# Kernel tuning notes

Hardware: AMD Instinct MI355X
Metric: run time of the kernel (lower is better)

The kernel has to match this reference:

```python
import jax, jax.numpy as jnp
import numpy as np

B, S, T, D, H, DF, E = 16, 1024, 512, 512, 8, 2048, 4
DH = D // H
EPS = 1e-5


def setup_inputs() -> dict:
    key = jax.random.key(0)
    ks = iter(jax.random.split(key, 64))

    def nrm(shape, scale=0.02):
        return jax.random.normal(next(ks), shape, dtype=jnp.float32) * scale

    inp = {
        "x": jax.random.normal(next(ks), (B, S, D), dtype=jnp.float32),
        "cross": jax.random.normal(next(ks), (B, T, D), dtype=jnp.float32),
    }
    for p in ("sa", "ca"):
        for w in ("wq", "wk", "wv", "wo"):
            inp[f"{p}_{w}"] = nrm((D, D))
            inp[f"{p}_b{w[1]}"] = jnp.zeros((D,), jnp.float32)
    inp["gate_w"] = nrm((D, E))
    inp["gate_b"] = jnp.zeros((E,), jnp.float32)
    inp["exp_w1"] = nrm((E, D, DF))
    inp["exp_b1"] = jnp.zeros((E, DF), jnp.float32)
    inp["exp_w2"] = nrm((E, DF, D))
    inp["exp_b2"] = jnp.zeros((E, D), jnp.float32)
    for i in (1, 2, 3):
        inp[f"n{i}_g"] = jnp.ones((D,), jnp.float32)
        inp[f"n{i}_b"] = jnp.zeros((D,), jnp.float32)
    return inp


def layer_norm(x, g, b):
    m = x.mean(-1, keepdims=True)
    v = x.var(-1, keepdims=True)
    return (x - m) * jax.lax.rsqrt(v + EPS) * g + b


def mha(q_in, kv_in, wq, bq, wk, bk, wv, bv, wo, bo, causal):
    Bq, Sq, _ = q_in.shape
    Sk = kv_in.shape[1]
    q = (q_in @ wq + bq).reshape(Bq, Sq, H, DH)
    k = (kv_in @ wk + bk).reshape(Bq, Sk, H, DH)
    v = (kv_in @ wv + bv).reshape(Bq, Sk, H, DH)
    scores = jnp.einsum('bshd,bthd->bhst', q, k) / jnp.sqrt(jnp.float32(DH))
    if causal:
        mask = jnp.tril(jnp.ones((Sq, Sk), dtype=bool))
        scores = jnp.where(mask, scores, jnp.float32(-1e9))
    attn = jax.nn.softmax(scores, axis=-1)
    out = jnp.einsum('bhst,bthd->bshd', attn, v).reshape(Bq, Sq, D)
    return out @ wo + bo


def moe_ffn(x, gw, gb, w1, b1, w2, b2):
    gates = jax.nn.softmax(x @ gw + gb, axis=-1)            # [B,S,E]
    h = jax.nn.relu(jnp.einsum('bsd,edf->bsef', x, w1) + b1)  # [B,S,E,DF]
    yo = jnp.einsum('bsef,efd->bsed', h, w2) + b2            # [B,S,E,D]
    y = jnp.einsum('bse,bsed->bsd', gates, yo)
    imp = gates.mean((0, 1))                                 # importance per expert
    aux = jnp.float32(E) * jnp.sum(imp * imp)                # load-balance penalty
    return y, aux


def reference(x, cross,
              sa_wq, sa_bq, sa_wk, sa_bk, sa_wv, sa_bv, sa_wo, sa_bo,
              ca_wq, ca_bq, ca_wk, ca_bk, ca_wv, ca_bv, ca_wo, ca_bo,
              gate_w, gate_b, exp_w1, exp_b1, exp_w2, exp_b2,
              n1_g, n1_b, n2_g, n2_b, n3_g, n3_b):
    # dropout is identity in eval mode
    x = x + mha(x, x, sa_wq, sa_bq, sa_wk, sa_bk, sa_wv, sa_bv, sa_wo, sa_bo, causal=True)
    x = layer_norm(x, n1_g, n1_b)
    x = x + mha(x, cross, ca_wq, ca_bq, ca_wk, ca_bk, ca_wv, ca_bv, ca_wo, ca_bo, causal=False)
    x = layer_norm(x, n2_g, n2_b)
    y, aux_loss = moe_ffn(x, gate_w, gate_b, exp_w1, exp_b1, exp_w2, exp_b2)
    out = layer_norm(x + y, n3_g, n3_b)
    return out, aux_loss
```

## Files before the change

### kernel.cpp

```cpp
#include <hip/hip_runtime.h>
#include <stdint.h>
#include <stddef.h>

typedef unsigned short bf16u;
typedef __attribute__((ext_vector_type(8))) short short8;
typedef __attribute__((ext_vector_type(4))) float f32x4;

__device__ __forceinline__ bf16u f2bf(float f) {
  union { float f; unsigned u; } v; v.f = f;
  unsigned r = v.u + 0x7FFFu + ((v.u >> 16) & 1u);
  return (bf16u)(r >> 16);
}

#define GL16(g, l) __builtin_amdgcn_global_load_lds( \
    (const __attribute__((address_space(1))) unsigned int*)(g), \
    (__attribute__((address_space(3))) unsigned int*)(l), 16, 0, 0)

enum { EPI_BF16 = 0, EPI_RELU_GATE = 1, EPI_QKV = 2, EPI_RES = 3, EPI_F32ACC = 4, EPI_KV = 5 };

template<int EPI>
__global__ __launch_bounds__(256, 3) void gemm_k(
    const bf16u* __restrict__ A, int LDA,
    const bf16u* __restrict__ BT, int LDB,
    const float* __restrict__ bias, const float* __restrict__ res,
    const float* __restrict__ gates,
    bf16u* __restrict__ o1, bf16u* __restrict__ o2, bf16u* __restrict__ o3,
    float* __restrict__ of,
    int N, int K, int slog, int egate0, int firste)
{
  __shared__ bf16u Ab[2][128 * 32];
  __shared__ bf16u Bb[2][128 * 32];
  const int tid = threadIdx.x, lane = tid & 63, w = tid >> 6;
  const int wm = w >> 1, wn = w & 1;
  const int cpx = gridDim.x >> 3;
  const int bid = (blockIdx.x & 7) * cpx + (blockIdx.x >> 3);
  const int nbt = N >> 7;
  const int mt = bid / nbt, nt = bid - mt * nbt;
  const int bm = mt << 7, bn = nt << 7;

  const int srow = lane >> 2;
  const int scol = (lane & 3) << 3;
  const bf16u* ap0 = A + (size_t)(bm + w * 16 + srow) * LDA + scol;
  const bf16u* ap1 = ap0 + (size_t)64 * LDA;
  const bf16u* bp0 = BT + (size_t)(bn + w * 16 + srow) * LDB + scol;
  const bf16u* bp1 = bp0 + (size_t)64 * LDB;

  f32x4 acc[4][4] = {};
  const int NT = K >> 5;

  GL16(ap0, &Ab[0][w * 512]);
  GL16(ap1, &Ab[0][(4 + w) * 512]);
  GL16(bp0, &Bb[0][w * 512]);
  GL16(bp1, &Bb[0][(4 + w) * 512]);
  __syncthreads();

  const int rl = lane & 15, kg = (lane >> 4) << 3;
  int cur = 0;
  for (int kt = 0; kt < NT; ++kt) {
    if (kt + 1 < NT) {
      const int ko = (kt + 1) << 5;
      const int nb = cur ^ 1;
      GL16(ap0 + ko, &Ab[nb][w * 512]);
      GL16(ap1 + ko, &Ab[nb][(4 + w) * 512]);
      GL16(bp0 + ko, &Bb[nb][w * 512]);
      GL16(bp1 + ko, &Bb[nb][(4 + w) * 512]);
    }
    short8 af[4], bfv[4];
    #pragma unroll
    for (int i = 0; i < 4; ++i)
      af[i] = *(const short8*)&Ab[cur][(wm * 64 + i * 16 + rl) * 32 + kg];
    #pragma unroll
    for (int j = 0; j < 4; ++j)
      bfv[j] = *(const short8*)&Bb[cur][(wn * 64 + j * 16 + rl) * 32 + kg];
    #pragma unroll
    for (int i = 0; i < 4; ++i)
      #pragma unroll
      for (int j = 0; j < 4; ++j)
        acc[i][j] = __builtin_amdgcn_mfma_f32_16x16x32_bf16(af[i], bfv[j], acc[i][j], 0, 0, 0);
    __syncthreads();
    cur ^= 1;
  }

  const int r0 = bm + wm * 64, c0 = bn + wn * 64;
  const int rsub = (lane >> 4) << 2;
  #pragma unroll
  for (int j = 0; j < 4; ++j) {
    const int col = c0 + j * 16 + rl;
    const float bs = bias ? bias[col] : 0.f;
    #pragma unroll
    for (int i = 0; i < 4; ++i) {
      const f32x4 v = acc[i][j];
      #pragma unroll
      for (int jj = 0; jj < 4; ++jj) {
        const int row = r0 + i * 16 + rsub + jj;
        const float val = v[jj] + bs;
        if (EPI == EPI_BF16) {
          o1[(size_t)row * N + col] = f2bf(val);
        } else if (EPI == EPI_RELU_GATE) {
          const float g = gates[(size_t)row * 4 + egate0 + (col >> 11)];
          o1[(size_t)row * N + col] = f2bf(g * (val > 0.f ? val : 0.f));
        } else if (EPI == EPI_QKV) {
          if (col < 512) o1[(size_t)row * 512 + col] = f2bf(val);
          else if (col < 1024) o2[(size_t)row * 512 + col - 512] = f2bf(val);
          else {
            const int c = col - 1024;
            const int b_ = row >> slog, t_ = row & ((1 << slog) - 1);
            o3[(((size_t)(b_ * 8 + (c >> 6)) << 6) + (size_t)(c & 63)) * ((size_t)1 << slog) + t_] = f2bf(val);
          }
        } else if (EPI == EPI_KV) {
          if (col < 512) o2[(size_t)row * 512 + col] = f2bf(val);
          else {
            const int c = col - 512;
            const int b_ = row >> slog, t_ = row & ((1 << slog) - 1);
            o3[(((size_t)(b_ * 8 + (c >> 6)) << 6) + (size_t)(c & 63)) * ((size_t)1 << slog) + t_] = f2bf(val);
          }
        } else if (EPI == EPI_RES) {
          of[(size_t)row * N + col] = res[(size_t)row * N + col] + val;
        } else {
          const size_t oi = (size_t)row * N + col;
          of[oi] = firste ? val : (of[oi] + val);
        }
      }
    }
  }
}

template<bool CAUSAL>
__global__ __launch_bounds__(256, 4) void attn_k(
    const bf16u* __restrict__ Q, const bf16u* __restrict__ Kg,
    const bf16u* __restrict__ VT, bf16u* __restrict__ O,
    int Sq, int Sk)
{
  __shared__ bf16u Kl[2][64 * 64];
  __shared__ bf16u Vl[2][64 * 64];
  __shared__ bf16u Pl[64 * 64];
  const int nqt = Sq >> 6;
  const int cpx = gridDim.x >> 3;
  const int bid = (blockIdx.x & 7) * cpx + (blockIdx.x >> 3);
  const int bh = bid / nqt;
  int qt = bid - bh * nqt;
  if (CAUSAL) qt = nqt - 1 - qt;
  const int b = bh >> 3, h = bh & 7;
  const int tid = threadIdx.x, lane = tid & 63, w = tid >> 6;
  const int rl = lane & 15, g4 = lane >> 4;

  const int qrow = qt * 64 + w * 16 + rl;
  const bf16u* qp = Q + (size_t)(b * Sq + qrow) * 512 + h * 64 + g4 * 8;
  const short8 qf0 = *(const short8*)qp;
  const short8 qf1 = *(const short8*)(qp + 32);

  f32x4 oacc[4] = {};
  float ml = -1e30f, ll = 0.f;
  const int KT = CAUSAL ? (qt + 1) : (Sk >> 6);

  const int str = tid >> 2, stc = tid & 3;
  const int sw_st = (str & 7) << 4;
  const bf16u* kq = Kg + (size_t)(b * Sk + str) * 512 + h * 64 + stc * 8;
  const bf16u* vq = VT + (size_t)(bh * 64 + str) * Sk + stc * 8;
  const int lo0 = str * 128 + ((stc * 16) ^ sw_st);
  const int lo1 = str * 128 + ((stc * 16 + 64) ^ sw_st);

  const int qr = w * 16 + rl;
  char* const pbase = (char*)Pl + qr * 128;
  const int swq = (qr & 7) << 4;

  {
    const short8 k0 = *(const short8*)kq;
    const short8 k1 = *(const short8*)(kq + 32);
    const short8 v0 = *(const short8*)vq;
    const short8 v1 = *(const short8*)(vq + 32);
    *(short8*)((char*)Kl[0] + lo0) = k0;
    *(short8*)((char*)Kl[0] + lo1) = k1;
    *(short8*)((char*)Vl[0] + lo0) = v0;
    *(short8*)((char*)Vl[0] + lo1) = v1;
  }
  __syncthreads();

  int cur = 0;
  for (int kt = 0; kt < KT; ++kt) {
    short8 nk0, nk1, nv0, nv1;
    const bool pre = (kt + 1 < KT);
    if (pre) {
      const bf16u* ks = kq + (size_t)(kt + 1) * 64 * 512;
      const bf16u* vs = vq + (kt + 1) * 64;
      nk0 = *(const short8*)ks;
      nk1 = *(const short8*)(ks + 32);
      nv0 = *(const short8*)vs;
      nv1 = *(const short8*)(vs + 32);
    }

    const bf16u* Kc = Kl[cur];
    const bf16u* Vc = Vl[cur];
    f32x4 st[4] = {};
    #pragma unroll
    for (int mi = 0; mi < 4; ++mi) {
      const int kr = mi * 16 + rl;
      const char* kb_ = (const char*)Kc + kr * 128;
      const int sw = (kr & 7) << 4;
      const short8 kf0 = *(const short8*)(kb_ + ((g4 * 16) ^ sw));
      const short8 kf1 = *(const short8*)(kb_ + ((g4 * 16 + 64) ^ sw));
      st[mi] = __builtin_amdgcn_mfma_f32_16x16x32_bf16(kf0, qf0, st[mi], 0, 0, 0);
      st[mi] = __builtin_amdgcn_mfma_f32_16x16x32_bf16(kf1, qf1, st[mi], 0, 0, 0);
    }

    const float SC = 0.125f * 1.44269504f;
    float sv[16];
    float pm = -1e30f;
    if (CAUSAL && kt == qt) {
      const int qg = qt * 64 + qr;
      #pragma unroll
      for (int mi = 0; mi < 4; ++mi)
        #pragma unroll
        for (int jj = 0; jj < 4; ++jj) {
          float s = st[mi][jj] * SC;
          const int kgi = kt * 64 + mi * 16 + g4 * 4 + jj;
          if (kgi > qg) s = -1e30f;
          sv[mi * 4 + jj] = s;
          pm = fmaxf(pm, s);
        }
    } else {
      #pragma unroll
      for (int mi = 0; mi < 4; ++mi)
        #pragma unroll
        for (int jj = 0; jj < 4; ++jj) {
          const float s = st[mi][jj] * SC;
          sv[mi * 4 + jj] = s;
          pm = fmaxf(pm, s);
        }
    }
    pm = fmaxf(pm, __shfl_xor(pm, 16));
    pm = fmaxf(pm, __shfl_xor(pm, 32));
    const float mnew = fmaxf(ml, pm);
    const float alpha = exp2f(ml - mnew);
    float ps = 0.f;
    bf16u pb[16];
    #pragma unroll
    for (int ii = 0; ii < 16; ++ii) {
      const float p = exp2f(sv[ii] - mnew);
      ps += p;
      pb[ii] = f2bf(p);
    }
    ps += __shfl_xor(ps, 16);
    ps += __shfl_xor(ps, 32);
    ll = ll * alpha + ps;
    ml = mnew;

    #pragma unroll
    for (int jj = 0; jj < 4; ++jj) {
      const float aj = __shfl(alpha, g4 * 4 + jj);
      #pragma unroll
      for (int ni = 0; ni < 4; ++ni) oacc[ni][jj] *= aj;
    }

    #pragma unroll
    for (int mi = 0; mi < 4; ++mi) {
      #pragma unroll
      for (int jp = 0; jp < 2; ++jp) {
        const unsigned pk = (unsigned)pb[mi * 4 + jp * 2] | ((unsigned)pb[mi * 4 + jp * 2 + 1] << 16);
        const int kx2 = mi * 32 + g4 * 8 + jp * 4;
        *(unsigned*)(pbase + (kx2 ^ swq)) = pk;
      }
    }
    asm volatile("s_waitcnt lgkmcnt(0)" ::: "memory");
    #pragma unroll
    for (int ks = 0; ks < 2; ++ks) {
      const short8 pf = *(const short8*)(pbase + ((g4 * 16 + ks * 64) ^ swq));
      #pragma unroll
      for (int ni = 0; ni < 4; ++ni) {
        const int vr = ni * 16 + rl;
        const short8 vf = *(const short8*)((const char*)Vc + vr * 128 + ((g4 * 16 + ks * 64) ^ ((vr & 7) << 4)));
        oacc[ni] = __builtin_amdgcn_mfma_f32_16x16x32_bf16(pf, vf, oacc[ni], 0, 0, 0);
      }
    }

    if (pre) {
      const int nb = cur ^ 1;
      *(short8*)((char*)Kl[nb] + lo0) = nk0;
      *(short8*)((char*)Kl[nb] + lo1) = nk1;
      *(short8*)((char*)Vl[nb] + lo0) = nv0;
      *(short8*)((char*)Vl[nb] + lo1) = nv1;
    }
    __syncthreads();
    cur ^= 1;
  }

  #pragma unroll
  for (int jj = 0; jj < 4; ++jj) {
    const float lj = __shfl(ll, g4 * 4 + jj);
    const float inv = 1.f / lj;
    const int row = qt * 64 + w * 16 + g4 * 4 + jj;
    #pragma unroll
    for (int ni = 0; ni < 4; ++ni)
      O[(size_t)(b * Sq + row) * 512 + h * 64 + ni * 16 + rl] = f2bf(oacc[ni][jj] * inv);
  }
}

template<bool ADD, bool BOUT, bool GATE>
__global__ __launch_bounds__(256, 4) void ln_k(
    const float* __restrict__ X, const float* __restrict__ Y,
    const float* __restrict__ gam, const float* __restrict__ bet,
    float* __restrict__ outf, bf16u* __restrict__ outb,
    const float* __restrict__ gw, const float* __restrict__ gb,
    float* __restrict__ gates, float* __restrict__ imp)
{
  __shared__ float sh[4];
  const int tid = threadIdx.x;
  if (GATE) {
    if (tid < 4) sh[tid] = 0.f;
    __syncthreads();
  }
  const int row = blockIdx.x * 4 + (tid >> 6);
  const int lane = tid & 63;
  const float* xp = X + (size_t)row * 512 + lane * 8;
  float v[8];
  {
    const float4 t0 = *(const float4*)xp;
    const float4 t1 = *(const float4*)(xp + 4);
    v[0] = t0.x; v[1] = t0.y; v[2] = t0.z; v[3] = t0.w;
    v[4] = t1.x; v[5] = t1.y; v[6] = t1.z; v[7] = t1.w;
  }
  if (ADD) {
    const float* yp = Y + (size_t)row * 512 + lane * 8;
    const float4 t0 = *(const float4*)yp;
    const float4 t1 = *(const float4*)(yp + 4);
    v[0] += t0.x; v[1] += t0.y; v[2] += t0.z; v[3] += t0.w;
    v[4] += t1.x; v[5] += t1.y; v[6] += t1.z; v[7] += t1.w;
  }
  float s = 0.f, q = 0.f;
  #pragma unroll
  for (int i = 0; i < 8; ++i) { s += v[i]; q += v[i] * v[i]; }
  #pragma unroll
  for (int off = 1; off < 64; off <<= 1) {
    s += __shfl_xor(s, off);
    q += __shfl_xor(q, off);
  }
  const float mean = s * (1.f / 512.f);
  const float var = q * (1.f / 512.f) - mean * mean;
  const float rs = rsqrtf(var + 1e-5f);
  float o[8];
  #pragma unroll
  for (int i = 0; i < 8; ++i)
    o[i] = (v[i] - mean) * rs * gam[lane * 8 + i] + bet[lane * 8 + i];
  float* op = outf + (size_t)row * 512 + lane * 8;
  *(float4*)op = make_float4(o[0], o[1], o[2], o[3]);
  *(float4*)(op + 4) = make_float4(o[4], o[5], o[6], o[7]);
  if (BOUT) {
    union { bf16u u[8]; short8 v8; } pk;
    #pragma unroll
    for (int i = 0; i < 8; ++i) pk.u[i] = f2bf(o[i]);
    *(short8*)(outb + (size_t)row * 512 + lane * 8) = pk.v8;
  }
  if (GATE) {
    float a0 = 0.f, a1 = 0.f, a2 = 0.f, a3 = 0.f;
    #pragma unroll
    for (int i = 0; i < 8; ++i) {
      const float4 wv = *(const float4*)(gw + (lane * 8 + i) * 4);
      a0 += o[i] * wv.x; a1 += o[i] * wv.y; a2 += o[i] * wv.z; a3 += o[i] * wv.w;
    }
    #pragma unroll
    for (int off = 1; off < 64; off <<= 1) {
      a0 += __shfl_xor(a0, off); a1 += __shfl_xor(a1, off);
      a2 += __shfl_xor(a2, off); a3 += __shfl_xor(a3, off);
    }
    if (lane == 0) {
      a0 += gb[0]; a1 += gb[1]; a2 += gb[2]; a3 += gb[3];
      const float m = fmaxf(fmaxf(a0, a1), fmaxf(a2, a3));
      const float e0 = exp2f((a0 - m) * 1.44269504f);
      const float e1 = exp2f((a1 - m) * 1.44269504f);
      const float e2 = exp2f((a2 - m) * 1.44269504f);
      const float e3 = exp2f((a3 - m) * 1.44269504f);
      const float inv = 1.f / (e0 + e1 + e2 + e3);
      float* gr = gates + (size_t)row * 4;
      const float g0 = e0 * inv, g1 = e1 * inv, g2 = e2 * inv, g3 = e3 * inv;
      gr[0] = g0; gr[1] = g1; gr[2] = g2; gr[3] = g3;
      atomicAdd(&sh[0], g0); atomicAdd(&sh[1], g1);
      atomicAdd(&sh[2], g2); atomicAdd(&sh[3], g3);
    }
    __syncthreads();
    if (tid < 4) atomicAdd(&imp[tid], sh[tid]);
  }
}

__global__ __launch_bounds__(256, 4) void ln_final_k(
    const float* __restrict__ X, const float* __restrict__ Y,
    const float* __restrict__ gates, const float* __restrict__ b2,
    const float* __restrict__ gam, const float* __restrict__ bet,
    float* __restrict__ outf, const float* __restrict__ imp,
    float* __restrict__ auxout)
{
  if (blockIdx.x == 0 && threadIdx.x == 0) {
    float s = 0.f;
    #pragma unroll
    for (int e = 0; e < 4; ++e) { const float v = imp[e] * (1.f / 16384.f); s += v * v; }
    auxout[0] = 4.f * s;
  }
  const int row = blockIdx.x * 4 + (threadIdx.x >> 6);
  const int lane = threadIdx.x & 63;
  const float4 gv4 = *(const float4*)(gates + (size_t)row * 4);
  float v[8];
  {
    const float* xp = X + (size_t)row * 512 + lane * 8;
    const float* yp = Y + (size_t)row * 512 + lane * 8;
    const float4 t0 = *(const float4*)xp;
    const float4 t1 = *(const float4*)(xp + 4);
    const float4 u0 = *(const float4*)yp;
    const float4 u1 = *(const float4*)(yp + 4);
    v[0] = t0.x + u0.x; v[1] = t0.y + u0.y; v[2] = t0.z + u0.z; v[3] = t0.w + u0.w;
    v[4] = t1.x + u1.x; v[5] = t1.y + u1.y; v[6] = t1.z + u1.z; v[7] = t1.w + u1.w;
  }
  #pragma unroll
  for (int e = 0; e < 4; ++e) {
    const float ge = e == 0 ? gv4.x : e == 1 ? gv4.y : e == 2 ? gv4.z : gv4.w;
    const float4 b0 = *(const float4*)(b2 + e * 512 + lane * 8);
    const float4 b1 = *(const float4*)(b2 + e * 512 + lane * 8 + 4);
    v[0] += ge * b0.x; v[1] += ge * b0.y; v[2] += ge * b0.z; v[3] += ge * b0.w;
    v[4] += ge * b1.x; v[5] += ge * b1.y; v[6] += ge * b1.z; v[7] += ge * b1.w;
  }
  float s = 0.f, q = 0.f;
  #pragma unroll
  for (int i = 0; i < 8; ++i) { s += v[i]; q += v[i] * v[i]; }
  #pragma unroll
  for (int off = 1; off < 64; off <<= 1) {
    s += __shfl_xor(s, off);
    q += __shfl_xor(q, off);
  }
  const float mean = s * (1.f / 512.f);
  const float var = q * (1.f / 512.f) - mean * mean;
  const float rs = rsqrtf(var + 1e-5f);
  float* op = outf + (size_t)row * 512 + lane * 8;
  float o[8];
  #pragma unroll
  for (int i = 0; i < 8; ++i)
    o[i] = (v[i] - mean) * rs * gam[lane * 8 + i] + bet[lane * 8 + i];
  *(float4*)op = make_float4(o[0], o[1], o[2], o[3]);
  *(float4*)(op + 4) = make_float4(o[4], o[5], o[6], o[7]);
}

__global__ __launch_bounds__(256, 4) void conv_k(const float* __restrict__ in, bf16u* __restrict__ out) {
  const size_t i = ((size_t)blockIdx.x * 256 + threadIdx.x) * 8;
  const float4 a = *(const float4*)(in + i);
  const float4 b = *(const float4*)(in + i + 4);
  union { bf16u u[8]; short8 v; } pk;
  pk.u[0] = f2bf(a.x); pk.u[1] = f2bf(a.y); pk.u[2] = f2bf(a.z); pk.u[3] = f2bf(a.w);
  pk.u[4] = f2bf(b.x); pk.u[5] = f2bf(b.y); pk.u[6] = f2bf(b.z); pk.u[7] = f2bf(b.w);
  *(short8*)(out + i) = pk.v;
}

struct P8 { const float* w[8]; };

__global__ __launch_bounds__(256, 4) void trans8_k(
    P8 ps, bf16u* __restrict__ WT0, int K, int N)
{
  const float* W = ps.w[blockIdx.z];
  bf16u* WT = WT0 + (size_t)blockIdx.z * K * N;
  __shared__ float t[32][33];
  const int tx = threadIdx.x & 31, ty = threadIdx.x >> 5;
  const int n0 = blockIdx.x * 32, k0 = blockIdx.y * 32;
  #pragma unroll
  for (int i = 0; i < 4; ++i)
    t[ty + i * 8][tx] = W[(size_t)(k0 + ty + i * 8) * N + n0 + tx];
  __syncthreads();
  #pragma unroll
  for (int i = 0; i < 4; ++i)
    WT[(size_t)(n0 + ty + i * 8) * K + k0 + tx] = f2bf(t[tx][ty + i * 8]);
}

__global__ __launch_bounds__(256, 4) void trans_s_k(
    const float* __restrict__ W0, size_t wstride,
    bf16u* __restrict__ WT0, size_t tstride, int K, int N)
{
  const float* W = W0 + (size_t)blockIdx.z * wstride;
  bf16u* WT = WT0 + (size_t)blockIdx.z * tstride;
  __shared__ float t[32][33];
  const int tx = threadIdx.x & 31, ty = threadIdx.x >> 5;
  const int n0 = blockIdx.x * 32, k0 = blockIdx.y * 32;
  #pragma unroll
  for (int i = 0; i < 4; ++i)
    t[ty + i * 8][tx] = W[(size_t)(k0 + ty + i * 8) * N + n0 + tx];
  __syncthreads();
  #pragma unroll
  for (int i = 0; i < 4; ++i)
    WT[(size_t)(n0 + ty + i * 8) * K + k0 + tx] = f2bf(t[tx][ty + i * 8]);
}

extern "C" void kernel_launch(void* const* d_in, const int* in_sizes, int n_in,
                              void* d_out, int out_size, void* d_ws, size_t ws_size,
                              hipStream_t stream)
{
  const int B = 16, S = 1024, T = 512, D = 512, DF = 2048, E = 4;
  const int M = B * S;
  const int Mc = B * T;
  (void)in_sizes; (void)n_in; (void)out_size;

  const float* x      = (const float*)d_in[0];
  const float* cross  = (const float*)d_in[1];
  const float* gate_w = (const float*)d_in[18];
  const float* gate_b = (const float*)d_in[19];
  const float* exp_w1 = (const float*)d_in[20];
  const float* exp_b1 = (const float*)d_in[21];
  const float* exp_w2 = (const float*)d_in[22];
  const float* exp_b2 = (const float*)d_in[23];

  char* p = (char*)d_ws;
  auto alloc = [&](size_t bytes) -> char* {
    char* r = p;
    p += (bytes + 255) & ~(size_t)255;
    return r;
  };
  bf16u* w1T   = (bf16u*)alloc((size_t)E * DF * D * 2);
  bf16u* w2T   = (bf16u*)alloc((size_t)D * E * DF * 2);
  float* xf    = (float*)alloc((size_t)M * D * 4);
  bf16u* x2b   = (bf16u*)alloc((size_t)M * D * 2);
  float* gates = (float*)alloc((size_t)M * 4 * 4);
  float* imp   = (float*)alloc(256);
  float* y     = (float*)alloc((size_t)M * D * 4);
  float* qkvb  = (float*)alloc(1536 * 4);
  float* kvb   = (float*)alloc(1024 * 4);

  char* upool = p;
  bf16u* xb  = (bf16u*)upool;
  bf16u* crb = xb  + (size_t)M * D;
  bf16u* wT  = crb + (size_t)Mc * D;
  bf16u* qb  = wT  + (size_t)8 * D * D;
  bf16u* kb  = qb  + (size_t)M * D;
  bf16u* vTb = kb  + (size_t)M * D;
  bf16u* ao  = vTb + (size_t)M * D;
  const size_t attnPool = ((size_t)M * D * 5 + (size_t)Mc * D + (size_t)8 * D * D) * 2;
  bf16u* hbuf = (bf16u*)upool;
  const size_t persistent = (size_t)(upool - (char*)d_ws);
  const size_t perE = (size_t)M * DF * 2;
  const size_t rem = ws_size > persistent ? ws_size - persistent : 0;
  const int EC = (rem >= 4 * perE && rem >= attnPool) ? 4
               : (rem >= 2 * perE && rem >= attnPool) ? 2 : 1;

  hipMemsetAsync(imp, 0, 32, stream);
  hipMemcpyAsync(qkvb,        d_in[3], 512 * 4, hipMemcpyDeviceToDevice, stream);
  hipMemcpyAsync(qkvb + 512,  d_in[5], 512 * 4, hipMemcpyDeviceToDevice, stream);
  hipMemcpyAsync(qkvb + 1024, d_in[7], 512 * 4, hipMemcpyDeviceToDevice, stream);
  hipMemcpyAsync(kvb,         d_in[13], 512 * 4, hipMemcpyDeviceToDevice, stream);
  hipMemcpyAsync(kvb + 512,   d_in[15], 512 * 4, hipMemcpyDeviceToDevice, stream);

  conv_k<<<(M * D) / 2048, 256, 0, stream>>>(x, xb);
  conv_k<<<(Mc * D) / 2048, 256, 0, stream>>>(cross, crb);
  {
    P8 ps;
    for (int i = 0; i < 8; ++i) ps.w[i] = (const float*)d_in[2 + 2 * i];
    trans8_k<<<dim3(D / 32, D / 32, 8), 256, 0, stream>>>(ps, wT, D, D);
  }
  trans_s_k<<<dim3(DF / 32, D / 32, 4), 256, 0, stream>>>(
      exp_w1, (size_t)D * DF, w1T, (size_t)DF * D, D, DF);
  trans_s_k<<<dim3(D / 32, (E * DF) / 32, 1), 256, 0, stream>>>(
      exp_w2, 0, w2T, 0, E * DF, D);

  const int gATT = B * 8 * (S / 64);

  gemm_k<EPI_QKV><<<(M / 128) * 12, 256, 0, stream>>>(
      xb, 512, wT, 512, qkvb, nullptr, nullptr, qb, kb, vTb, nullptr, 1536, 512, 10, 0, 0);
  attn_k<true><<<gATT, 256, 0, stream>>>(qb, kb, vTb, ao, S, S);
  gemm_k<EPI_RES><<<(M / 128) * 4, 256, 0, stream>>>(
      ao, 512, wT + 3 * (size_t)D * D, 512, (const float*)d_in[9], x, nullptr,
      nullptr, nullptr, nullptr, xf, 512, 512, 0, 0, 0);
  ln_k<false, true, false><<<M / 4, 256, 0, stream>>>(
      xf, nullptr, (const float*)d_in[24], (const float*)d_in[25], xf, x2b,
      nullptr, nullptr, nullptr, nullptr);

  gemm_k<EPI_BF16><<<(M / 128) * 4, 256, 0, stream>>>(
      x2b, 512, wT + 4 * (size_t)D * D, 512, (const float*)d_in[11], nullptr, nullptr,
      qb, nullptr, nullptr, nullptr, 512, 512, 0, 0, 0);
  gemm_k<EPI_KV><<<(Mc / 128) * 8, 256, 0, stream>>>(
      crb, 512, wT + 5 * (size_t)D * D, 512, kvb, nullptr, nullptr,
      nullptr, kb, vTb, nullptr, 1024, 512, 9, 0, 0);
  attn_k<false><<<gATT, 256, 0, stream>>>(qb, kb, vTb, ao, S, T);
  gemm_k<EPI_RES><<<(M / 128) * 4, 256, 0, stream>>>(
      ao, 512, wT + 7 * (size_t)D * D, 512, (const float*)d_in[17], xf, nullptr,
      nullptr, nullptr, nullptr, xf, 512, 512, 0, 0, 0);
  ln_k<false, true, true><<<M / 4, 256, 0, stream>>>(
      xf, nullptr, (const float*)d_in[26], (const float*)d_in[27], xf, x2b,
      gate_w, gate_b, gates, imp);

  const int NC = E / EC;
  const int Nh = EC * DF;
  for (int c = 0; c < NC; ++c) {
    gemm_k<EPI_RELU_GATE><<<(M / 128) * (Nh / 128), 256, 0, stream>>>(
        x2b, 512, w1T + (size_t)c * Nh * D, 512, exp_b1 + (size_t)c * Nh, nullptr, gates,
        hbuf, nullptr, nullptr, nullptr, Nh, 512, 0, c * EC, 0);
    gemm_k<EPI_F32ACC><<<(M / 128) * 4, 256, 0, stream>>>(
        hbuf, Nh, w2T + (size_t)c * Nh, E * DF, nullptr, nullptr, nullptr,
        nullptr, nullptr, nullptr, y, 512, Nh, 0, 0, c == 0 ? 1 : 0);
  }
  ln_final_k<<<M / 4, 256, 0, stream>>>(
      xf, y, gates, exp_b2, (const float*)d_in[28], (const float*)d_in[29],
      (float*)d_out, imp, (float*)d_out + (size_t)M * D);
}
```

Before: 869.4 us.

## Keep residual stream in bf16 and raise MFMA wave priority in attention

Stores the residual activations between layers as bf16 instead of fp32. The residual GEMM epilogues now emit bf16, the LayerNorm kernels read bf16 and write only a bf16 output, and a new EPI_RESB epilogue adds a bf16 residual. This removes the fp32 residual writes and reads and the dual-format LN outputs, cutting memory traffic between kernels. It also wraps the attention MFMA blocks in s_setprio so the matrix-multiply sections get scheduling priority. The risk is lower accuracy in the residual path, with bf16 rounding applied before each LayerNorm and the final output.

Measured after the change: 888.8 us. +2.2%, slower.

```diff
diff --git a/kernel.cpp b/kernel.cpp
--- a/kernel.cpp
+++ b/kernel.cpp
@@ -11,19 +11,23 @@
   unsigned r = v.u + 0x7FFFu + ((v.u >> 16) & 1u);
   return (bf16u)(r >> 16);
 }
+__device__ __forceinline__ float bf2f(bf16u u) {
+  union { unsigned u; float f; } v; v.u = (unsigned)u << 16; return v.f;
+}
 
 #define GL16(g, l) __builtin_amdgcn_global_load_lds( \
     (const __attribute__((address_space(1))) unsigned int*)(g), \
     (__attribute__((address_space(3))) unsigned int*)(l), 16, 0, 0)
 
-enum { EPI_BF16 = 0, EPI_RELU_GATE = 1, EPI_QKV = 2, EPI_RES = 3, EPI_F32ACC = 4, EPI_KV = 5 };
+enum { EPI_BF16 = 0, EPI_RELU_GATE = 1, EPI_QKV = 2, EPI_RES = 3, EPI_RESB = 4,
+       EPI_F32ACC = 5, EPI_KV = 6 };
 
 template<int EPI>
 __global__ __launch_bounds__(256, 3) void gemm_k(
     const bf16u* __restrict__ A, int LDA,
     const bf16u* __restrict__ BT, int LDB,
     const float* __restrict__ bias, const float* __restrict__ res,
-    const float* __restrict__ gates,
+    const bf16u* __restrict__ resb, const float* __restrict__ gates,
     bf16u* __restrict__ o1, bf16u* __restrict__ o2, bf16u* __restrict__ o3,
     float* __restrict__ of,
     int N, int K, int slog, int egate0, int firste)
@@ -115,7 +119,9 @@
             o3[(((size_t)(b_ * 8 + (c >> 6)) << 6) + (size_t)(c & 63)) * ((size_t)1 << slog) + t_] = f2bf(val);
           }
         } else if (EPI == EPI_RES) {
-          of[(size_t)row * N + col] = res[(size_t)row * N + col] + val;
+          o1[(size_t)row * N + col] = f2bf(res[(size_t)row * N + col] + val);
+        } else if (EPI == EPI_RESB) {
+          o1[(size_t)row * N + col] = f2bf(bf2f(resb[(size_t)row * N + col]) + val);
         } else {
           const size_t oi = (size_t)row * N + col;
           of[oi] = firste ? val : (of[oi] + val);
@@ -192,6 +198,7 @@
     const bf16u* Kc = Kl[cur];
     const bf16u* Vc = Vl[cur];
     f32x4 st[4] = {};
+    __builtin_amdgcn_s_setprio(1);
     #pragma unroll
     for (int mi = 0; mi < 4; ++mi) {
       const int kr = mi * 16 + rl;
@@ -202,6 +209,7 @@
       st[mi] = __builtin_amdgcn_mfma_f32_16x16x32_bf16(kf0, qf0, st[mi], 0, 0, 0);
       st[mi] = __builtin_amdgcn_mfma_f32_16x16x32_bf16(kf1, qf1, st[mi], 0, 0, 0);
     }
+    __builtin_amdgcn_s_setprio(0);
 
     const float SC = 0.125f * 1.44269504f;
     float sv[16];
@@ -262,6 +270,7 @@
       }
     }
     asm volatile("s_waitcnt lgkmcnt(0)" ::: "memory");
+    __builtin_amdgcn_s_setprio(1);
     #pragma unroll
     for (int ks = 0; ks < 2; ++ks) {
       const short8 pf = *(const short8*)(pbase + ((g4 * 16 + ks * 64) ^ swq));
@@ -272,6 +281,7 @@
         oacc[ni] = __builtin_amdgcn_mfma_f32_16x16x32_bf16(pf, vf, oacc[ni], 0, 0, 0);
       }
     }
+    __builtin_amdgcn_s_setprio(0);
 
     if (pre) {
       const int nb = cur ^ 1;
@@ -295,11 +305,11 @@
   }
 }
 
-template<bool ADD, bool BOUT, bool GATE>
+template<bool GATE>
 __global__ __launch_bounds__(256, 4) void ln_k(
-    const float* __restrict__ X, const float* __restrict__ Y,
+    const bf16u* __restrict__ X,
     const float* __restrict__ gam, const float* __restrict__ bet,
-    float* __restrict__ outf, bf16u* __restrict__ outb,
+    bf16u* __restrict__ outb,
     const float* __restrict__ gw, const float* __restrict__ gb,
     float* __restrict__ gates, float* __restrict__ imp)
 {
@@ -311,21 +321,10 @@
   }
   const int row = blockIdx.x * 4 + (tid >> 6);
   const int lane = tid & 63;
-  const float* xp = X + (size_t)row * 512 + lane * 8;
+  const short8 xv = *(const short8*)(X + (size_t)row * 512 + lane * 8);
   float v[8];
-  {
-    const float4 t0 = *(const float4*)xp;
-    const float4 t1 = *(const float4*)(xp + 4);
-    v[0] = t0.x; v[1] = t0.y; v[2] = t0.z; v[3] = t0.w;
-    v[4] = t1.x; v[5] = t1.y; v[6] = t1.z; v[7] = t1.w;
-  }
-  if (ADD) {
-    const float* yp = Y + (size_t)row * 512 + lane * 8;
-    const float4 t0 = *(const float4*)yp;
-    const float4 t1 = *(const float4*)(yp + 4);
-    v[0] += t0.x; v[1] += t0.y; v[2] += t0.z; v[3] += t0.w;
-    v[4] += t1.x; v[5] += t1.y; v[6] += t1.z; v[7] += t1.w;
-  }
+  #pragma unroll
+  for (int i = 0; i < 8; ++i) v[i] = bf2f((bf16u)xv[i]);
   float s = 0.f, q = 0.f;
   #pragma unroll
   for (int i = 0; i < 8; ++i) { s += v[i]; q += v[i] * v[i]; }
@@ -341,15 +340,10 @@
   #pragma unroll
   for (int i = 0; i < 8; ++i)
     o[i] = (v[i] - mean) * rs * gam[lane * 8 + i] + bet[lane * 8 + i];
-  float* op = outf + (size_t)row * 512 + lane * 8;
-  *(float4*)op = make_float4(o[0], o[1], o[2], o[3]);
-  *(float4*)(op + 4) = make_float4(o[4], o[5], o[6], o[7]);
-  if (BOUT) {
-    union { bf16u u[8]; short8 v8; } pk;
-    #pragma unroll
-    for (int i = 0; i < 8; ++i) pk.u[i] = f2bf(o[i]);
-    *(short8*)(outb + (size_t)row * 512 + lane * 8) = pk.v8;
-  }
+  union { bf16u u[8]; short8 v8; } pk;
+  #pragma unroll
+  for (int i = 0; i < 8; ++i) pk.u[i] = f2bf(o[i]);
+  *(short8*)(outb + (size_t)row * 512 + lane * 8) = pk.v8;
   if (GATE) {
     float a0 = 0.f, a1 = 0.f, a2 = 0.f, a3 = 0.f;
     #pragma unroll
@@ -382,7 +376,7 @@
 }
 
 __global__ __launch_bounds__(256, 4) void ln_final_k(
-    const float* __restrict__ X, const float* __restrict__ Y,
+    const bf16u* __restrict__ X, const float* __restrict__ Y,
     const float* __restrict__ gates, const float* __restrict__ b2,
     const float* __restrict__ gam, const float* __restrict__ bet,
     float* __restrict__ outf, const float* __restrict__ imp,
@@ -397,16 +391,16 @@
   const int row = blockIdx.x * 4 + (threadIdx.x >> 6);
   const int lane = threadIdx.x & 63;
   const float4 gv4 = *(const float4*)(gates + (size_t)row * 4);
+  const short8 xv = *(const short8*)(X + (size_t)row * 512 + lane * 8);
   float v[8];
   {
-    const float* xp = X + (size_t)row * 512 + lane * 8;
     const float* yp = Y + (size_t)row * 512 + lane * 8;
-    const float4 t0 = *(const float4*)xp;
-    const float4 t1 = *(const float4*)(xp + 4);
     const float4 u0 = *(const float4*)yp;
     const float4 u1 = *(const float4*)(yp + 4);
-    v[0] = t0.x + u0.x; v[1] = t0.y + u0.y; v[2] = t0.z + u0.z; v[3] = t0.w + u0.w;
-    v[4] = t1.x + u1.x; v[5] = t1.y + u1.y; v[6] = t1.z + u1.z; v[7] = t1.w + u1.w;
+    v[0] = bf2f((bf16u)xv[0]) + u0.x; v[1] = bf2f((bf16u)xv[1]) + u0.y;
+    v[2] = bf2f((bf16u)xv[2]) + u0.z; v[3] = bf2f((bf16u)xv[3]) + u0.w;
+    v[4] = bf2f((bf16u)xv[4]) + u1.x; v[5] = bf2f((bf16u)xv[5]) + u1.y;
+    v[6] = bf2f((bf16u)xv[6]) + u1.z; v[7] = bf2f((bf16u)xv[7]) + u1.w;
   }
   #pragma unroll
   for (int e = 0; e < 4; ++e) {
@@ -509,8 +503,8 @@
   };
   bf16u* w1T   = (bf16u*)alloc((size_t)E * DF * D * 2);
   bf16u* w2T   = (bf16u*)alloc((size_t)D * E * DF * 2);
-  float* xf    = (float*)alloc((size_t)M * D * 4);
   bf16u* x2b   = (bf16u*)alloc((size_t)M * D * 2);
+  bf16u* x3b   = (bf16u*)alloc((size_t)M * D * 2);
   float* gates = (float*)alloc((size_t)M * 4 * 4);
   float* imp   = (float*)alloc(256);
   float* y     = (float*)alloc((size_t)M * D * 4);
@@ -525,6 +519,8 @@
   bf16u* kb  = qb  + (size_t)M * D;
   bf16u* vTb = kb  + (size_t)M * D;
   bf16u* ao  = vTb + (size_t)M * D;
+  bf16u* x1b  = xb;
+  bf16u* x3pb = crb;
   const size_t attnPool = ((size_t)M * D * 5 + (size_t)Mc * D + (size_t)8 * D * D) * 2;
   bf16u* hbuf = (bf16u*)upool;
   const size_t persistent = (size_t)(upool - (char*)d_ws);
@@ -555,40 +551,40 @@
   const int gATT = B * 8 * (S / 64);
 
   gemm_k<EPI_QKV><<<(M / 128) * 12, 256, 0, stream>>>(
-      xb, 512, wT, 512, qkvb, nullptr, nullptr, qb, kb, vTb, nullptr, 1536, 512, 10, 0, 0);
+      xb, 512, wT, 512, qkvb, nullptr, nullptr, nullptr, qb, kb, vTb, nullptr, 1536, 512, 10, 0, 0);
   attn_k<true><<<gATT, 256, 0, stream>>>(qb, kb, vTb, ao, S, S);
   gemm_k<EPI_RES><<<(M / 128) * 4, 256, 0, stream>>>(
-      ao, 512, wT + 3 * (size_t)D * D, 512, (const float*)d_in[9], x, nullptr,
-      nullptr, nullptr, nullptr, xf, 512, 512, 0, 0, 0);
-  ln_k<false, true, false><<<M / 4, 256, 0, stream>>>(
-      xf, nullptr, (const float*)d_in[24], (const float*)d_in[25], xf, x2b,
+      ao, 512, wT + 3 * (size_t)D * D, 512, (const float*)d_in[9], x, nullptr, nullptr,
+      x1b, nullptr, nullptr, nullptr, 512, 512, 0, 0, 0);
+  ln_k<false><<<M / 4, 256, 0, stream>>>(
+      x1b, (const float*)d_in[24], (const float*)d_in[25], x2b,
       nullptr, nullptr, nullptr, nullptr);
 
   gemm_k<EPI_BF16><<<(M / 128) * 4, 256, 0, stream>>>(
-      x2b, 512, wT + 4 * (size_t)D * D, 512, (const float*)d_in[11], nullptr, nullptr,
+      x2b, 512, wT + 4 * (size_t)D * D, 512, (const float*)d_in[11], nullptr, nullptr, nullptr,
       qb, nullptr, nullptr, nullptr, 512, 512, 0, 0, 0);
   gemm_k<EPI_KV><<<(Mc / 128) * 8, 256, 0, stream>>>(
-      crb, 512, wT + 5 * (size_t)D * D, 512, kvb, nullptr, nullptr,
+      crb, 512, wT + 5 * (size_t)D * D, 512, kvb, nullptr, nullptr, nullptr,
       nullptr, kb, vTb, nullptr, 1024, 512, 9, 0, 0);
   attn_k<false><<<gATT, 256, 0, stream>>>(qb, kb, vTb, ao, S, T);
-  gemm_k<EPI_RES><<<(M / 128) * 4, 256, 0, stream>>>(
-      ao, 512, wT + 7 * (size_t)D * D, 512, (const float*)d_in[17], xf, nullptr,
-      nullptr, nullptr, nullptr, xf, 512, 512, 0, 0, 0);
-  ln_k<false, true, true><<<M / 4, 256, 0, stream>>>(
-      xf, nullptr, (const float*)d_in[26], (const float*)d_in[27], xf, x2b,
+  gemm_k<EPI_RESB><<<(M / 128) * 4, 256, 0, stream>>>(
+      ao, 512, wT + 7 * (size_t)D * D, 512, (const float*)d_in[17], nullptr, x2b, nullptr,
+      x3pb, nullptr, nullptr, nullptr, 512, 512, 0, 0, 0);
+  ln_k<true><<<M / 4, 256, 0, stream>>>(
+      x3pb, (const float*)d_in[26], (const float*)d_in[27], x3b,
       gate_w, gate_b, gates, imp);
 
   const int NC = E / EC;
   const int Nh = EC * DF;
   for (int c = 0; c < NC; ++c) {
     gemm_k<EPI_RELU_GATE><<<(M / 128) * (Nh / 128), 256, 0, stream>>>(
-        x2b, 512, w1T + (size_t)c * Nh * D, 512, exp_b1 + (size_t)c * Nh, nullptr, gates,
+        x3b, 512, w1T + (size_t)c * Nh * D, 512, exp_b1 + (size_t)c * Nh, nullptr, nullptr, gates,
         hbuf, nullptr, nullptr, nullptr, Nh, 512, 0, c * EC, 0);
     gemm_k<EPI_F32ACC><<<(M / 128) * 4, 256, 0, stream>>>(
-        hbuf, Nh, w2T + (size_t)c * Nh, E * DF, nullptr, nullptr, nullptr,
+        hbuf, Nh, w2T + (size_t)c * Nh, E * DF, nullptr, nullptr, nullptr, nullptr,
         nullptr, nullptr, nullptr, y, 512, Nh, 0, 0, c == 0 ? 1 : 0);
   }
   ln_final_k<<<M / 4, 256, 0, stream>>>(
-      xf, y, gates, exp_b2, (const float*)d_in[28], (const float*)d_in[29],
+      x3b, y, gates, exp_b2, (const float*)d_in[28], (const float*)d_in[29],
       (float*)d_out, imp, (float*)d_out + (size_t)M * D);
 }
```
